# Kernel tuning notes

Hardware: AMD Instinct MI355X
Metric: run time of the kernel (lower is better)

The kernel has to match this reference:

```python
import jax, jax.numpy as jnp
import numpy as np

B, L, K, H = 2, 2048, 48, 128
NUM_IN = 2 * H          # h_E (H) + gathered h_V (H)
SCALE = 30.0            # EncLayer scale
LN_EPS = 1e-5


def _linear_params(key, fan_in, fan_out):
    kw, kb = jax.random.split(key)
    s = 1.0 / np.sqrt(fan_in)
    W = jax.random.uniform(kw, (fan_in, fan_out), minval=-s, maxval=s, dtype=jnp.float32)
    b = jax.random.uniform(kb, (fan_out,), minval=-s, maxval=s, dtype=jnp.float32)
    return W, b


def setup_inputs() -> dict:
    key = jax.random.key(0)
    ks = jax.random.split(key, 12)
    h_V = jax.random.normal(ks[0], (B, L, H), dtype=jnp.float32)
    h_E = jax.random.normal(ks[1], (B, L, K, H), dtype=jnp.float32)
    E_idx = jax.random.randint(ks[2], (B, L, K), 0, L, dtype=jnp.int64)
    mask_V = jnp.ones((B, L), dtype=jnp.float32)
    mask_attend = jnp.ones((B, L, K), dtype=jnp.float32)

    W1, b1 = _linear_params(ks[3], H + NUM_IN, H)
    W2, b2 = _linear_params(ks[4], H, H)
    W3, b3 = _linear_params(ks[5], H, H)
    W11, b11 = _linear_params(ks[6], H + NUM_IN, H)
    W12, b12 = _linear_params(ks[7], H, H)
    W13, b13 = _linear_params(ks[8], H, H)
    Wi, bi = _linear_params(ks[9], H, 4 * H)   # PositionWiseFeedForward W_in
    Wo, bo = _linear_params(ks[10], 4 * H, H)  # W_out

    ln = lambda: (jnp.ones((H,), jnp.float32), jnp.zeros((H,), jnp.float32))
    ln1_s, ln1_b = ln(); ln2_s, ln2_b = ln(); ln3_s, ln3_b = ln()

    return dict(h_V=h_V, h_E=h_E, E_idx=E_idx, mask_V=mask_V, mask_attend=mask_attend,
                W1=W1, b1=b1, W2=W2, b2=b2, W3=W3, b3=b3,
                W11=W11, b11=b11, W12=W12, b12=b12, W13=W13, b13=b13,
                Wi=Wi, bi=bi, Wo=Wo, bo=bo,
                ln1_s=ln1_s, ln1_b=ln1_b, ln2_s=ln2_s, ln2_b=ln2_b,
                ln3_s=ln3_s, ln3_b=ln3_b)


def gather_nodes(nodes, idx):
    # nodes: [B, L, H], idx: [B, L, K] -> [B, L, K, H]
    b, l, h = nodes.shape
    flat = idx.reshape(b, -1)  # [B, L*K]
    g = jnp.take_along_axis(nodes, flat[..., None], axis=1)  # [B, L*K, H]
    return g.reshape(b, idx.shape[1], idx.shape[2], h)


def layer_norm(x, scale, bias):
    mu = jnp.mean(x, axis=-1, keepdims=True)
    var = jnp.mean((x - mu) ** 2, axis=-1, keepdims=True)
    return (x - mu) / jnp.sqrt(var + LN_EPS) * scale + bias


def gelu(x):
    return jax.nn.gelu(x, approximate=False)  # torch nn.GELU default (erf)


def enc_layer_forward(h_V, h_E, E_idx, mask_V, mask_attend, p):
    # --- node update: gather neighbors, concat, MLP, masked sum-reduce ---
    h_EV = jnp.concatenate([h_E, gather_nodes(h_V, E_idx)], axis=-1)        # [B,L,K,2H]
    h_V_exp = jnp.broadcast_to(h_V[:, :, None, :], h_EV.shape[:3] + (h_V.shape[-1],))
    h_EV = jnp.concatenate([h_V_exp, h_EV], axis=-1)                        # [B,L,K,3H]
    m = gelu(h_EV @ p['W1'] + p['b1'])
    m = gelu(m @ p['W2'] + p['b2'])
    m = m @ p['W3'] + p['b3']
    m = mask_attend[..., None] * m
    dh = jnp.sum(m, axis=-2) / SCALE                                        # [B,L,H]
    h_V = layer_norm(h_V + dh, p['ln1_s'], p['ln1_b'])
    # --- position-wise FFN ---
    dh = gelu(h_V @ p['Wi'] + p['bi']) @ p['Wo'] + p['bo']
    h_V = layer_norm(h_V + dh, p['ln2_s'], p['ln2_b'])
    h_V = mask_V[..., None] * h_V
    # --- edge update ---
    h_EV = jnp.concatenate([h_E, gather_nodes(h_V, E_idx)], axis=-1)
    h_V_exp = jnp.broadcast_to(h_V[:, :, None, :], h_EV.shape[:3] + (h_V.shape[-1],))
    h_EV = jnp.concatenate([h_V_exp, h_EV], axis=-1)
    m = gelu(h_EV @ p['W11'] + p['b11'])
    m = gelu(m @ p['W12'] + p['b12'])
    m = m @ p['W13'] + p['b13']
    h_E = layer_norm(h_E + m, p['ln3_s'], p['ln3_b'])
    return h_V, h_E


def reference(h_V, h_E, E_idx, mask_V, mask_attend,
              W1, b1, W2, b2, W3, b3, W11, b11, W12, b12, W13, b13,
              Wi, bi, Wo, bo, ln1_s, ln1_b, ln2_s, ln2_b, ln3_s, ln3_b):
    p = dict(W1=W1, b1=b1, W2=W2, b2=b2, W3=W3, b3=b3,
             W11=W11, b11=b11, W12=W12, b12=b12, W13=W13, b13=b13,
             Wi=Wi, bi=bi, Wo=Wo, bo=bo,
             ln1_s=ln1_s, ln1_b=ln1_b, ln2_s=ln2_s, ln2_b=ln2_b,
             ln3_s=ln3_s, ln3_b=ln3_b)
    return enc_layer_forward(h_V, h_E, E_idx, mask_V, mask_attend, p)
```

## Files before the change

### kernel.cpp

```cpp
#include <hip/hip_runtime.h>
#include <hip/hip_bf16.h>
#include <math.h>

typedef unsigned short u16;
typedef __attribute__((ext_vector_type(8))) short bf16x8;
typedef __attribute__((ext_vector_type(4))) float f32x4;
typedef __attribute__((ext_vector_type(4))) unsigned int uint4v;
typedef __attribute__((ext_vector_type(2))) unsigned int uint2v;
typedef __attribute__((ext_vector_type(4))) unsigned short u16x4;

#define BB 2
#define LL 2048
#define KN 48
#define HH 128
#define NBLK (BB*LL)
#define ST 136

#define WOFF      16
#define OFF_W1MT  (WOFF + 0)
#define OFF_W1ST  (WOFF + 16384)
#define OFF_W1GT  (WOFF + 32768)
#define OFF_W2T   (WOFF + 49152)
#define OFF_W3T   (WOFF + 65536)
#define OFF_W11MT (WOFF + 81920)
#define OFF_W11ST (WOFF + 98304)
#define OFF_W11GT (WOFF + 114688)
#define OFF_W12T  (WOFF + 131072)
#define OFF_W13T  (WOFF + 147456)
#define OFF_WIT   (WOFF + 163840)
#define OFF_WOT   (WOFF + 229376)
#define OFF_HV1   (WOFF + 294912)
#define OFF_Q1    (WOFF + 819200)
#define OFF_Q2    (WOFF + 1343488)
#define OFF_R1    (WOFF + 1867776)
#define OFF_R2    (WOFF + 2916352)
#define PREP_N    294912

__device__ __forceinline__ float b2f(u16 u){
    union { unsigned int i; float f; } v; v.i = ((unsigned int)u) << 16; return v.f;
}
__device__ __forceinline__ u16 f2b(float f){
    unsigned int x = __float_as_uint(f);
    unsigned int r = x + 0x7fffu + ((x >> 16) & 1u);
    return (u16)(r >> 16);
}
__device__ __forceinline__ unsigned int f2b2(float lo, float hi){
    unsigned int r;
    asm("v_cvt_pk_bf16_f32 %0, %1, %2" : "=v"(r) : "v"(lo), "v"(hi));
    return r;
}
__device__ __forceinline__ float gelu_f(float x){
    float ax = fabsf(x) * 0.70710678118654752f;
    float t  = __builtin_amdgcn_rcpf(fmaf(0.3275911f, ax, 1.0f));
    float e  = __builtin_amdgcn_exp2f(ax * ax * -1.4426950408889634f);
    float p  = fmaf(1.061405429f, t, -1.453152027f);
    p = fmaf(p, t, 1.421413741f);
    p = fmaf(p, t, -0.284496736f);
    p = fmaf(p, t, 0.254829592f);
    p = p * t;
    float erfv = fmaf(-p, e, 1.0f);
    float hx = 0.5f * x;
    return fmaf(fabsf(hx), erfv, hx);
}
__device__ __forceinline__ u16 ldb(const void* p, long i, int f32){
    return f32 ? f2b(((const float*)p)[i]) : ((const u16*)p)[i];
}
__device__ __forceinline__ float ldf(const void* p, long i, int f32){
    return f32 ? ((const float*)p)[i] : b2f(((const u16*)p)[i]);
}
__device__ __forceinline__ f32x4 ldf4(const void* p, long i, int f32){
    f32x4 r;
    if (f32){
        r = *(const f32x4*)((const float*)p + i);
    } else {
        u16x4 v = *(const u16x4*)((const u16*)p + i);
        r[0]=b2f(v[0]); r[1]=b2f(v[1]); r[2]=b2f(v[2]); r[3]=b2f(v[3]);
    }
    return r;
}
__device__ __forceinline__ void st4(void* p, long i, f32x4 v, int f32){
    if (f32){
        *(f32x4*)((float*)p + i) = v;
    } else {
        uint2v u; u.x = f2b2(v[0], v[1]); u.y = f2b2(v[2], v[3]);
        *(uint2v*)((u16*)p + i) = u;
    }
}
__device__ __forceinline__ void stage8(u16* dst, const void* src, long off, int f32){
    if (f32){
        const float* s = (const float*)src + off;
        f32x4 a = *(const f32x4*)(s);
        f32x4 b = *(const f32x4*)(s + 4);
        uint4v v;
        v.x = f2b2(a[0], a[1]); v.y = f2b2(a[2], a[3]);
        v.z = f2b2(b[0], b[1]); v.w = f2b2(b[2], b[3]);
        *(uint4v*)dst = v;
    } else {
        *(uint4v*)dst = *(const uint4v*)((const u16*)src + off);
    }
}
__device__ __forceinline__ int ld_idx(const void* p, int i, int i64){
    int v = i64 ? ((const int*)p)[2*i] : ((const int*)p)[i];
    return v & (LL - 1);
}

__global__ void detect_kernel(const void* ln1s, const void* maskV, const void* eidx, int* flags){
    if (threadIdx.x == 0){
        unsigned l0 = ((const unsigned*)ln1s)[0];
        unsigned m0 = ((const unsigned*)maskV)[0];
        int f32 = (l0 == 0x3F800000u || m0 == 0x3F800000u) ? 1 : 0;
        const int* e = (const int*)eidx;
        int orodd = 0, orlow = 0;
        for (int i = 1; i < 64; i += 2) orodd |= e[i];
        for (int i = 0; i < 64; i += 2) orlow |= e[i];
        flags[0] = f32;
        flags[1] = (orodd == 0 && orlow != 0) ? 1 : 0;
    }
}

__global__ void prep_kernel(const void* W1, const void* W2, const void* W3,
                            const void* W11, const void* W12, const void* W13,
                            const void* Wi, const void* Wo, u16* wsbase){
    const int f32 = ((const int*)wsbase)[0];
    int i = blockIdx.x * 256 + threadIdx.x;
    if (i < 16384){ int n = i >> 7, k = i & 127; wsbase[OFF_W1MT + i] = ldb(W1, (128 + k)*128 + n, f32); }
    else if (i < 32768){ int j = i - 16384;  int n = j >> 7, k = j & 127; wsbase[OFF_W1ST  + j] = ldb(W1, k*128 + n, f32); }
    else if (i < 49152){ int j = i - 32768;  int n = j >> 7, k = j & 127; wsbase[OFF_W1GT  + j] = ldb(W1, (256 + k)*128 + n, f32); }
    else if (i < 65536){ int j = i - 49152;  int n = j >> 7, k = j & 127; wsbase[OFF_W2T   + j] = ldb(W2, k*128 + n, f32); }
    else if (i < 81920){ int j = i - 65536;  int n = j >> 7, k = j & 127; wsbase[OFF_W3T   + j] = ldb(W3, k*128 + n, f32); }
    else if (i < 98304){ int j = i - 81920;  int n = j >> 7, k = j & 127; wsbase[OFF_W11MT + j] = ldb(W11, (128 + k)*128 + n, f32); }
    else if (i < 114688){ int j = i - 98304; int n = j >> 7, k = j & 127; wsbase[OFF_W11ST + j] = ldb(W11, k*128 + n, f32); }
    else if (i < 131072){ int j = i - 114688;int n = j >> 7, k = j & 127; wsbase[OFF_W11GT + j] = ldb(W11, (256 + k)*128 + n, f32); }
    else if (i < 147456){ int j = i - 131072;int n = j >> 7, k = j & 127; wsbase[OFF_W12T  + j] = ldb(W12, k*128 + n, f32); }
    else if (i < 163840){ int j = i - 147456;int n = j >> 7, k = j & 127; wsbase[OFF_W13T  + j] = ldb(W13, k*128 + n, f32); }
    else if (i < 229376){ int j = i - 163840; int h = j >> 7, c = j & 127; wsbase[OFF_WIT + j] = ldb(Wi, c*512 + h, f32); }
    else if (i < 294912){ int j = i - 229376; int c = j >> 9, h = j & 511; wsbase[OFF_WOT + j] = ldb(Wo, h*128 + c, f32); }
}

__global__ __launch_bounds__(256) void precomp_kernel(
    const void* __restrict__ src, const void* __restrict__ bias,
    u16* __restrict__ wsbase, long offWs, long offWg, long offQ, long offR)
{
    __shared__ alignas(16) u16 X[16 * ST];
    const int f32 = ((const int*)wsbase)[0];
    const int t = threadIdx.x, lane = t & 63, w = t >> 6;
    const int node0 = blockIdx.x * 16;
    const int r16 = lane & 15, q = lane >> 4, q8 = q * 8;

    {
        int row = t >> 4, ch = t & 15;
        stage8(X + row * ST + ch * 8, src, ((long)(node0 + row)) * HH + ch * 8, f32);
    }
    __syncthreads();

    const u16* bp = X + r16 * ST + q8;
#pragma unroll
    for (int half = 0; half < 2; half++){
        long offW = half ? offWg : offWs;
#pragma unroll
        for (int nt = 0; nt < 2; nt++){
            int wr = w * 32 + nt * 16 + r16;
            const u16* ap = wsbase + offW + (long)wr * 128 + q8;
            f32x4 acc; acc[0]=0.f; acc[1]=0.f; acc[2]=0.f; acc[3]=0.f;
#pragma unroll
            for (int kk = 0; kk < 4; kk++){
                bf16x8 av = *(const bf16x8*)(ap + kk * 32);
                bf16x8 bv = *(const bf16x8*)(bp + kk * 32);
                acc = __builtin_amdgcn_mfma_f32_16x16x32_bf16(av, bv, acc, 0, 0, 0);
            }
            int c0 = w * 32 + nt * 16 + q * 4;
            if (half == 0){
                f32x4 bc = ldf4(bias, c0, f32);
                float* Rf = (float*)(wsbase + offR);
                f32x4 rr; rr[0]=acc[0]+bc[0]; rr[1]=acc[1]+bc[1]; rr[2]=acc[2]+bc[2]; rr[3]=acc[3]+bc[3];
                *(f32x4*)(Rf + (long)(node0 + r16) * HH + c0) = rr;
            } else {
                uint2v u; u.x = f2b2(acc[0], acc[1]); u.y = f2b2(acc[2], acc[3]);
                *(uint2v*)(wsbase + offQ + (long)(node0 + r16) * HH + c0) = u;
            }
        }
    }
}

__device__ __forceinline__ void mfma_WB(const u16* Mls, const bf16x8* W,
                                        f32x4 acc[3], int lane){
    const int r16 = lane & 15;
    const int q8  = (lane >> 4) * 8;
    const u16* bp = Mls + r16 * ST + q8;
#pragma unroll
    for (int kk = 0; kk < 4; kk++){
        bf16x8 b0 = *(const bf16x8*)(bp + kk * 32);
        bf16x8 b1 = *(const bf16x8*)(bp + 16 * ST + kk * 32);
        bf16x8 b2 = *(const bf16x8*)(bp + 32 * ST + kk * 32);
        acc[0] = __builtin_amdgcn_mfma_f32_16x16x32_bf16(W[kk], b0, acc[0], 0, 0, 0);
        acc[1] = __builtin_amdgcn_mfma_f32_16x16x32_bf16(W[kk], b1, acc[1], 0, 0, 0);
        acc[2] = __builtin_amdgcn_mfma_f32_16x16x32_bf16(W[kk], b2, acc[2], 0, 0, 0);
    }
}

__device__ __forceinline__ void zero_acc3(f32x4 acc[3]){
#pragma unroll
    for (int m = 0; m < 3; m++){ acc[m][0]=0.f; acc[m][1]=0.f; acc[m][2]=0.f; acc[m][3]=0.f; }
}

__device__ __forceinline__ void init_accT(f32x4 acc[3], const u16* Qg, int lane, int w){
    const int r16 = lane & 15, q = lane >> 4;
    const int c0 = w * 16 + q * 4;
#pragma unroll
    for (int mt = 0; mt < 3; mt++){
        u16x4 v = *(const u16x4*)(Qg + (mt * 16 + r16) * ST + c0);
        acc[mt][0]=b2f(v[0]); acc[mt][1]=b2f(v[1]); acc[mt][2]=b2f(v[2]); acc[mt][3]=b2f(v[3]);
    }
}

__device__ __forceinline__ void store_T(f32x4 acc[3], u16* M, f32x4 bc4,
                                        int lane, int w, bool dogelu){
    const int r16 = lane & 15, q = lane >> 4;
    const int c0 = w * 16 + q * 4;
#pragma unroll
    for (int mt = 0; mt < 3; mt++){
        float v0 = acc[mt][0] + bc4[0], v1 = acc[mt][1] + bc4[1];
        float v2 = acc[mt][2] + bc4[2], v3 = acc[mt][3] + bc4[3];
        if (dogelu){ v0 = gelu_f(v0); v1 = gelu_f(v1); v2 = gelu_f(v2); v3 = gelu_f(v3); }
        uint2v u; u.x = f2b2(v0, v1); u.y = f2b2(v2, v3);
        *(uint2v*)(M + (mt * 16 + r16) * ST + c0) = u;
    }
}

__global__ __launch_bounds__(512, 6) void node_kernel(
    const void* __restrict__ hV, const void* __restrict__ hE, const void* __restrict__ Eidx,
    const void* __restrict__ maskA,
    const void* __restrict__ b2, const void* __restrict__ b3,
    const void* __restrict__ ln1s, const void* __restrict__ ln1b,
    u16* __restrict__ wsbase)
{
    __shared__ alignas(16) u16 A[KN * ST];
    __shared__ alignas(16) u16 Qg[KN * ST];
    __shared__ alignas(16) u16 M1[KN * ST];
    __shared__ float smask[KN];
    __shared__ alignas(16) float dh[HH];
    __shared__ float hv0f[HH];
    u16* M2 = A;

    const int f32 = ((const int*)wsbase)[0];
    const int i64 = ((const int*)wsbase)[1];
    const u16* ws = wsbase;
    const int t = threadIdx.x, lane = t & 63, w = t >> 6;
    const int bid = blockIdx.x;
    const int b = bid >> 11;
    const int r16 = lane & 15, q = lane >> 4, q8 = q * 8;
    const int wrow = w * 16 + r16;
    const int c0 = w * 16 + q * 4;

    bf16x8 B1[4];
    {
        const u16* bp = ws + OFF_W1MT + (long)wrow * 128 + q8;
#pragma unroll
        for (int k = 0; k < 4; k++) B1[k] = *(const bf16x8*)(bp + k * 32);
    }

    for (int i = t; i < 768; i += 512){
        int row = i >> 4, ch = i & 15;
        stage8(A + row * ST + ch * 8, hE, ((long)bid * KN + row) * HH + ch * 8, f32);
    }
    for (int i = t; i < 768; i += 512){
        int row = i >> 4, ch = i & 15;
        int nb = ld_idx(Eidx, bid * KN + row, i64);
        *(uint4v*)(Qg + row * ST + ch * 8) =
            *(const uint4v*)(ws + OFF_Q1 + ((long)b * LL + nb) * HH + ch * 8);
    }
    if (t < HH) hv0f[t] = ldf(hV, (long)bid * HH + t, f32);
    if (t < KN) smask[t] = ldf(maskA, bid * KN + t, f32);

    bf16x8 B2[4];
    {
        const u16* bp = ws + OFF_W2T + (long)wrow * 128 + q8;
#pragma unroll
        for (int k = 0; k < 4; k++) B2[k] = *(const bf16x8*)(bp + k * 32);
    }
    const f32x4 bc1 = *(const f32x4*)((const float*)(wsbase + OFF_R1) + (long)bid * HH + c0);
    __syncthreads();

    f32x4 acc[3];
    init_accT(acc, Qg, lane, w);
    __builtin_amdgcn_s_setprio(1);
    mfma_WB(A, B1, acc, lane);
    __builtin_amdgcn_s_setprio(0);
    store_T(acc, M1, bc1, lane, w, true);

    bf16x8 B3[4];
    {
        const u16* bp = ws + OFF_W3T + (long)wrow * 128 + q8;
#pragma unroll
        for (int k = 0; k < 4; k++) B3[k] = *(const bf16x8*)(bp + k * 32);
    }
    __syncthreads();

    zero_acc3(acc);
    __builtin_amdgcn_s_setprio(1);
    mfma_WB(M1, B2, acc, lane);
    __builtin_amdgcn_s_setprio(0);
    store_T(acc, M2, ldf4(b2, c0, f32), lane, w, true);
    __syncthreads();

    zero_acc3(acc);
    __builtin_amdgcn_s_setprio(1);
    mfma_WB(M2, B3, acc, lane);
    __builtin_amdgcn_s_setprio(0);

    {
        f32x4 b3v = ldf4(b3, c0, f32);
        f32x4 s; s[0]=0.f; s[1]=0.f; s[2]=0.f; s[3]=0.f;
#pragma unroll
        for (int mt = 0; mt < 3; mt++){
            float mk = smask[mt * 16 + r16];
#pragma unroll
            for (int j = 0; j < 4; j++) s[j] += mk * (acc[mt][j] + b3v[j]);
        }
#pragma unroll
        for (int off = 1; off <= 8; off <<= 1){
#pragma unroll
            for (int j = 0; j < 4; j++) s[j] += __shfl_xor(s[j], off);
        }
        if (r16 == 0) *(f32x4*)&dh[c0] = s;
    }
    __syncthreads();

    if (w == 0){
        float xa = hv0f[lane]      + dh[lane]      * (1.0f / 30.0f);
        float xb = hv0f[64 + lane] + dh[64 + lane] * (1.0f / 30.0f);
        float sum = xa + xb, sq = xa * xa + xb * xb;
#pragma unroll
        for (int off = 1; off < 64; off <<= 1){ sum += __shfl_xor(sum, off); sq += __shfl_xor(sq, off); }
        float mu = sum * (1.0f / 128.0f);
        float var = sq * (1.0f / 128.0f) - mu * mu;
        float rstd = rsqrtf(var + 1e-5f);
        wsbase[OFF_HV1 + (long)bid * HH + lane] =
            f2b((xa - mu) * rstd * ldf(ln1s, lane, f32) + ldf(ln1b, lane, f32));
        wsbase[OFF_HV1 + (long)bid * HH + 64 + lane] =
            f2b((xb - mu) * rstd * ldf(ln1s, 64 + lane, f32) + ldf(ln1b, 64 + lane, f32));
    }
}

__global__ __launch_bounds__(512, 6) void ffn_kernel(
    const void* __restrict__ maskV,
    const void* __restrict__ bi, const void* __restrict__ bo,
    const void* __restrict__ b11,
    const void* __restrict__ ln2s, const void* __restrict__ ln2b,
    u16* __restrict__ wsbase, void* __restrict__ dout)
{
    __shared__ alignas(16) u16 X[16 * 136];
    __shared__ alignas(16) u16 Hid[16 * 520];
    __shared__ alignas(16) float V[16 * 132];

    const int f32 = ((const int*)wsbase)[0];
    const u16* ws = wsbase;
    const u16* hv1 = wsbase + OFF_HV1;
    const int t = threadIdx.x, lane = t & 63, w = t >> 6;
    const int node0 = blockIdx.x * 16;
    const int r16 = lane & 15, q = lane >> 4, q8 = q * 8;
    const int c0 = w * 16 + q * 4;

    if (t < 256){
        int row = t >> 4, ch = t & 15;
        *(uint4v*)(X + row * 136 + ch * 8) =
            *(const uint4v*)(hv1 + (long)(node0 + row) * HH + ch * 8);
    }
    __syncthreads();

    f32x4 acc[4];
#pragma unroll
    for (int nt = 0; nt < 4; nt++){ acc[nt][0]=0.f; acc[nt][1]=0.f; acc[nt][2]=0.f; acc[nt][3]=0.f; }
    {
        const u16* bp = X + r16 * 136 + q8;
#pragma unroll
        for (int kk = 0; kk < 4; kk++){
            bf16x8 bv = *(const bf16x8*)(bp + kk * 32);
#pragma unroll
            for (int nt = 0; nt < 4; nt++){
                const u16* ap = ws + OFF_WIT + (long)(w * 64 + nt * 16 + r16) * 128 + kk * 32 + q8;
                bf16x8 av = *(const bf16x8*)ap;
                acc[nt] = __builtin_amdgcn_mfma_f32_16x16x32_bf16(av, bv, acc[nt], 0, 0, 0);
            }
        }
    }
#pragma unroll
    for (int nt = 0; nt < 4; nt++){
        int hc0 = w * 64 + nt * 16 + q * 4;
        f32x4 bc = ldf4(bi, hc0, f32);
        float g0 = gelu_f(acc[nt][0] + bc[0]), g1 = gelu_f(acc[nt][1] + bc[1]);
        float g2 = gelu_f(acc[nt][2] + bc[2]), g3 = gelu_f(acc[nt][3] + bc[3]);
        uint2v u; u.x = f2b2(g0, g1); u.y = f2b2(g2, g3);
        *(uint2v*)(Hid + r16 * 520 + hc0) = u;
    }
    __syncthreads();

    f32x4 acc2; acc2[0]=0.f; acc2[1]=0.f; acc2[2]=0.f; acc2[3]=0.f;
    {
        const u16* ap = ws + OFF_WOT + (long)(w * 16 + r16) * 512 + q8;
        const u16* bp = Hid + r16 * 520 + q8;
        __builtin_amdgcn_s_setprio(1);
#pragma unroll
        for (int kk = 0; kk < 16; kk++){
            bf16x8 av = *(const bf16x8*)(ap + kk * 32);
            bf16x8 bv = *(const bf16x8*)(bp + kk * 32);
            acc2 = __builtin_amdgcn_mfma_f32_16x16x32_bf16(av, bv, acc2, 0, 0, 0);
        }
        __builtin_amdgcn_s_setprio(0);
    }
    {
        f32x4 bo4 = ldf4(bo, c0, f32);
        u16x4 xr = *(const u16x4*)(X + r16 * 136 + c0);
        f32x4 vv;
        vv[0] = acc2[0] + bo4[0] + b2f(xr[0]);
        vv[1] = acc2[1] + bo4[1] + b2f(xr[1]);
        vv[2] = acc2[2] + bo4[2] + b2f(xr[2]);
        vv[3] = acc2[3] + bo4[3] + b2f(xr[3]);
        *(f32x4*)&V[r16 * 132 + c0] = vv;
    }
    __syncthreads();

    {
        int row = t >> 5, p = t & 31;
        f32x4 v = *(const f32x4*)&V[row * 132 + p * 4];
        float sum = v[0] + v[1] + v[2] + v[3];
        float sq = v[0]*v[0] + v[1]*v[1] + v[2]*v[2] + v[3]*v[3];
#pragma unroll
        for (int off = 1; off < 32; off <<= 1){ sum += __shfl_xor(sum, off); sq += __shfl_xor(sq, off); }
        float mu = sum * (1.0f / 128.0f);
        float var = sq * (1.0f / 128.0f) - mu * mu;
        float rstd = rsqrtf(var + 1e-5f);
        float mv = ldf(maskV, node0 + row, f32);
        f32x4 s4 = ldf4(ln2s, p * 4, f32), bb4 = ldf4(ln2b, p * 4, f32);
        f32x4 y;
#pragma unroll
        for (int j = 0; j < 4; j++) y[j] = ((v[j] - mu) * rstd * s4[j] + bb4[j]) * mv;
        st4(dout, (long)(node0 + row) * HH + p * 4, y, f32);
        uint2v u; u.x = f2b2(y[0], y[1]); u.y = f2b2(y[2], y[3]);
        *(uint2v*)(X + row * 136 + p * 4) = u;
    }
    __syncthreads();

    {
        const u16* bp = X + r16 * 136 + q8;
        f32x4 aR, aQ;
        aR[0]=0.f; aR[1]=0.f; aR[2]=0.f; aR[3]=0.f;
        aQ[0]=0.f; aQ[1]=0.f; aQ[2]=0.f; aQ[3]=0.f;
#pragma unroll
        for (int kk = 0; kk < 4; kk++){
            bf16x8 bv = *(const bf16x8*)(bp + kk * 32);
            bf16x8 avR = *(const bf16x8*)(ws + OFF_W11ST + (long)(w * 16 + r16) * 128 + kk * 32 + q8);
            bf16x8 avQ = *(const bf16x8*)(ws + OFF_W11GT + (long)(w * 16 + r16) * 128 + kk * 32 + q8);
            aR = __builtin_amdgcn_mfma_f32_16x16x32_bf16(avR, bv, aR, 0, 0, 0);
            aQ = __builtin_amdgcn_mfma_f32_16x16x32_bf16(avQ, bv, aQ, 0, 0, 0);
        }
        f32x4 b11v = ldf4(b11, c0, f32);
        float* Rf = (float*)(wsbase + OFF_R2);
        f32x4 rr;
#pragma unroll
        for (int j = 0; j < 4; j++) rr[j] = aR[j] + b11v[j];
        *(f32x4*)(Rf + (long)(node0 + r16) * HH + c0) = rr;
        uint2v u; u.x = f2b2(aQ[0], aQ[1]); u.y = f2b2(aQ[2], aQ[3]);
        *(uint2v*)(wsbase + OFF_Q2 + (long)(node0 + r16) * HH + c0) = u;
    }
}

__global__ __launch_bounds__(512, 6) void edge_kernel(
    const void* __restrict__ hE, const void* __restrict__ Eidx,
    const void* __restrict__ b12, const void* __restrict__ b13,
    const void* __restrict__ ln3s, const void* __restrict__ ln3b,
    u16* __restrict__ wsbase, void* __restrict__ dout)
{
    __shared__ alignas(16) u16 A[KN * ST];
    __shared__ alignas(16) u16 Qg[KN * ST];
    __shared__ alignas(16) u16 M1[KN * ST];
    __shared__ float rowsum[KN];
    __shared__ float rowsq[KN];
    u16* M2 = A;

    const int f32 = ((const int*)wsbase)[0];
    const int i64 = ((const int*)wsbase)[1];
    const u16* ws = wsbase;
    const int t = threadIdx.x, lane = t & 63, w = t >> 6;
    const int bid = blockIdx.x;
    const int b = bid >> 11;
    const int r16 = lane & 15, q = lane >> 4, q8 = q * 8;
    const int wrow = w * 16 + r16;
    const int c0 = w * 16 + q * 4;

    bf16x8 B1[4];
    {
        const u16* bp = ws + OFF_W11MT + (long)wrow * 128 + q8;
#pragma unroll
        for (int k = 0; k < 4; k++) B1[k] = *(const bf16x8*)(bp + k * 32);
    }

    for (int i = t; i < 768; i += 512){
        int row = i >> 4, ch = i & 15;
        stage8(A + row * ST + ch * 8, hE, ((long)bid * KN + row) * HH + ch * 8, f32);
    }
    for (int i = t; i < 768; i += 512){
        int row = i >> 4, ch = i & 15;
        int nb = ld_idx(Eidx, bid * KN + row, i64);
        *(uint4v*)(Qg + row * ST + ch * 8) =
            *(const uint4v*)(ws + OFF_Q2 + ((long)b * LL + nb) * HH + ch * 8);
    }
    if (t < KN){ rowsum[t] = 0.f; rowsq[t] = 0.f; }

    bf16x8 B2[4];
    {
        const u16* bp = ws + OFF_W12T + (long)wrow * 128 + q8;
#pragma unroll
        for (int k = 0; k < 4; k++) B2[k] = *(const bf16x8*)(bp + k * 32);
    }
    const f32x4 bc1 = *(const f32x4*)((const float*)(wsbase + OFF_R2) + (long)bid * HH + c0);
    __syncthreads();

    f32x4 acc[3];
    init_accT(acc, Qg, lane, w);
    __builtin_amdgcn_s_setprio(1);
    mfma_WB(A, B1, acc, lane);
    __builtin_amdgcn_s_setprio(0);
    store_T(acc, M1, bc1, lane, w, true);

    bf16x8 B3[4];
    {
        const u16* bp = ws + OFF_W13T + (long)wrow * 128 + q8;
#pragma unroll
        for (int k = 0; k < 4; k++) B3[k] = *(const bf16x8*)(bp + k * 32);
    }
    __syncthreads();

    zero_acc3(acc);
    __builtin_amdgcn_s_setprio(1);
    mfma_WB(M1, B2, acc, lane);
    __builtin_amdgcn_s_setprio(0);
    store_T(acc, M2, ldf4(b12, c0, f32), lane, w, true);
    __syncthreads();

    zero_acc3(acc);
    __builtin_amdgcn_s_setprio(1);
    mfma_WB(M2, B3, acc, lane);
    __builtin_amdgcn_s_setprio(0);

    f32x4 vals[3];
    {
        f32x4 b13v = ldf4(b13, c0, f32);
#pragma unroll
        for (int mt = 0; mt < 3; mt++){
            int r = mt * 16 + r16;
            f32x4 res = ldf4(hE, ((long)bid * KN + r) * HH + c0, f32);
#pragma unroll
            for (int j = 0; j < 4; j++) vals[mt][j] = acc[mt][j] + b13v[j] + res[j];
        }
    }
    {
        float s[3], ss[3];
#pragma unroll
        for (int mt = 0; mt < 3; mt++){
            s[mt]  = vals[mt][0] + vals[mt][1] + vals[mt][2] + vals[mt][3];
            ss[mt] = vals[mt][0]*vals[mt][0] + vals[mt][1]*vals[mt][1]
                   + vals[mt][2]*vals[mt][2] + vals[mt][3]*vals[mt][3];
            s[mt]  += __shfl_xor(s[mt], 16);  s[mt]  += __shfl_xor(s[mt], 32);
            ss[mt] += __shfl_xor(ss[mt], 16); ss[mt] += __shfl_xor(ss[mt], 32);
        }
        if (lane < 16){
#pragma unroll
            for (int mt = 0; mt < 3; mt++){
                atomicAdd(&rowsum[mt * 16 + lane], s[mt]);
                atomicAdd(&rowsq[mt * 16 + lane], ss[mt]);
            }
        }
    }
    __syncthreads();
    if (t < KN){
        float mu = rowsum[t] * (1.0f / 128.0f);
        float var = rowsq[t] * (1.0f / 128.0f) - mu * mu;
        rowsum[t] = mu;
        rowsq[t] = rsqrtf(var + 1e-5f);
    }
    __syncthreads();

    {
        long ebase = (long)BB * LL * HH;
        f32x4 g4 = ldf4(ln3s, c0, f32), be4 = ldf4(ln3b, c0, f32);
#pragma unroll
        for (int mt = 0; mt < 3; mt++){
            int r = mt * 16 + r16;
            float mu = rowsum[r], rs = rowsq[r];
            f32x4 y;
#pragma unroll
            for (int j = 0; j < 4; j++) y[j] = (vals[mt][j] - mu) * rs * g4[j] + be4[j];
            st4(dout, ebase + ((long)bid * KN + r) * HH + c0, y, f32);
        }
    }
}

extern "C" void kernel_launch(void* const* d_in, const int* in_sizes, int n_in,
                              void* d_out, int out_size, void* d_ws, size_t ws_size,
                              hipStream_t stream) {
    const void* hV    = d_in[0];
    const void* hE    = d_in[1];
    const void* Eidx  = d_in[2];
    const void* maskV = d_in[3];
    const void* maskA = d_in[4];
    const void* W1  = d_in[5];  const void* b1  = d_in[6];
    const void* W2  = d_in[7];  const void* b2  = d_in[8];
    const void* W3  = d_in[9];  const void* b3  = d_in[10];
    const void* W11 = d_in[11]; const void* b11 = d_in[12];
    const void* W12 = d_in[13]; const void* b12 = d_in[14];
    const void* W13 = d_in[15]; const void* b13 = d_in[16];
    const void* Wi  = d_in[17]; const void* bi  = d_in[18];
    const void* Wo  = d_in[19]; const void* bo  = d_in[20];
    const void* ln1s = d_in[21]; const void* ln1b = d_in[22];
    const void* ln2s = d_in[23]; const void* ln2b = d_in[24];
    const void* ln3s = d_in[25]; const void* ln3b = d_in[26];

    u16* ws = (u16*)d_ws;

    detect_kernel<<<1, 64, 0, stream>>>(ln1s, maskV, Eidx, (int*)d_ws);
    prep_kernel<<<(PREP_N + 255) / 256, 256, 0, stream>>>(W1, W2, W3, W11, W12, W13, Wi, Wo, ws);
    precomp_kernel<<<NBLK / 16, 256, 0, stream>>>(hV, b1, ws,
                                                  (long)OFF_W1ST, (long)OFF_W1GT,
                                                  (long)OFF_Q1, (long)OFF_R1);
    node_kernel<<<NBLK, 512, 0, stream>>>(hV, hE, Eidx, maskA,
                                          b2, b3, ln1s, ln1b, ws);
    ffn_kernel<<<NBLK / 16, 512, 0, stream>>>(maskV, bi, bo, b11, ln2s, ln2b, ws, d_out);
    edge_kernel<<<NBLK, 512, 0, stream>>>(hE, Eidx, b12, b13,
                                          ln3s, ln3b, ws, d_out);
}
```

Baseline: 373.1 us.

## Gather neighbor projections directly into accumulators and halve node tiles in small kernels

```diff
diff --git a/kernel.cpp b/kernel.cpp
--- a/kernel.cpp
+++ b/kernel.cpp
@@ -137,19 +137,24 @@
     else if (i < 294912){ int j = i - 229376; int c = j >> 9, h = j & 511; wsbase[OFF_WOT + j] = ldb(Wo, h*128 + c, f32); }
 }
 
-__global__ __launch_bounds__(256) void precomp_kernel(
+__global__ __launch_bounds__(256, 8) void precomp_kernel(
     const void* __restrict__ src, const void* __restrict__ bias,
     u16* __restrict__ wsbase, long offWs, long offWg, long offQ, long offR)
 {
     __shared__ alignas(16) u16 X[16 * ST];
     const int f32 = ((const int*)wsbase)[0];
     const int t = threadIdx.x, lane = t & 63, w = t >> 6;
-    const int node0 = blockIdx.x * 16;
+    const int node0 = blockIdx.x * 8;
     const int r16 = lane & 15, q = lane >> 4, q8 = q * 8;
 
     {
         int row = t >> 4, ch = t & 15;
-        stage8(X + row * ST + ch * 8, src, ((long)(node0 + row)) * HH + ch * 8, f32);
+        if (t < 128){
+            stage8(X + row * ST + ch * 8, src, ((long)(node0 + row)) * HH + ch * 8, f32);
+        } else {
+            uint4v z; z.x=0u; z.y=0u; z.z=0u; z.w=0u;
+            *(uint4v*)(X + row * ST + ch * 8) = z;
+        }
     }
     __syncthreads();
 
@@ -169,14 +174,16 @@
                 acc = __builtin_amdgcn_mfma_f32_16x16x32_bf16(av, bv, acc, 0, 0, 0);
             }
             int c0 = w * 32 + nt * 16 + q * 4;
-            if (half == 0){
-                f32x4 bc = ldf4(bias, c0, f32);
-                float* Rf = (float*)(wsbase + offR);
-                f32x4 rr; rr[0]=acc[0]+bc[0]; rr[1]=acc[1]+bc[1]; rr[2]=acc[2]+bc[2]; rr[3]=acc[3]+bc[3];
-                *(f32x4*)(Rf + (long)(node0 + r16) * HH + c0) = rr;
-            } else {
-                uint2v u; u.x = f2b2(acc[0], acc[1]); u.y = f2b2(acc[2], acc[3]);
-                *(uint2v*)(wsbase + offQ + (long)(node0 + r16) * HH + c0) = u;
+            if (r16 < 8){
+                if (half == 0){
+                    f32x4 bc = ldf4(bias, c0, f32);
+                    float* Rf = (float*)(wsbase + offR);
+                    f32x4 rr; rr[0]=acc[0]+bc[0]; rr[1]=acc[1]+bc[1]; rr[2]=acc[2]+bc[2]; rr[3]=acc[3]+bc[3];
+                    *(f32x4*)(Rf + (long)(node0 + r16) * HH + c0) = rr;
+                } else {
+                    uint2v u; u.x = f2b2(acc[0], acc[1]); u.y = f2b2(acc[2], acc[3]);
+                    *(uint2v*)(wsbase + offQ + (long)(node0 + r16) * HH + c0) = u;
+                }
             }
         }
     }
@@ -203,12 +210,14 @@
     for (int m = 0; m < 3; m++){ acc[m][0]=0.f; acc[m][1]=0.f; acc[m][2]=0.f; acc[m][3]=0.f; }
 }
 
-__device__ __forceinline__ void init_accT(f32x4 acc[3], const u16* Qg, int lane, int w){
+__device__ __forceinline__ void init_accG(f32x4 acc[3], const u16* Qbase, const void* Eidx,
+                                          int bid, int b, int i64, int lane, int w){
     const int r16 = lane & 15, q = lane >> 4;
     const int c0 = w * 16 + q * 4;
 #pragma unroll
     for (int mt = 0; mt < 3; mt++){
-        u16x4 v = *(const u16x4*)(Qg + (mt * 16 + r16) * ST + c0);
+        int nb = ld_idx(Eidx, bid * KN + mt * 16 + r16, i64);
+        u16x4 v = *(const u16x4*)(Qbase + ((long)b * LL + nb) * HH + c0);
         acc[mt][0]=b2f(v[0]); acc[mt][1]=b2f(v[1]); acc[mt][2]=b2f(v[2]); acc[mt][3]=b2f(v[3]);
     }
 }
@@ -235,7 +244,6 @@
     u16* __restrict__ wsbase)
 {
     __shared__ alignas(16) u16 A[KN * ST];
-    __shared__ alignas(16) u16 Qg[KN * ST];
     __shared__ alignas(16) u16 M1[KN * ST];
     __shared__ float smask[KN];
     __shared__ alignas(16) float dh[HH];
@@ -252,6 +260,9 @@
     const int wrow = w * 16 + r16;
     const int c0 = w * 16 + q * 4;
 
+    f32x4 acc[3];
+    init_accG(acc, ws + OFF_Q1, Eidx, bid, b, i64, lane, w);
+
     bf16x8 B1[4];
     {
         const u16* bp = ws + OFF_W1MT + (long)wrow * 128 + q8;
@@ -263,12 +274,6 @@
         int row = i >> 4, ch = i & 15;
         stage8(A + row * ST + ch * 8, hE, ((long)bid * KN + row) * HH + ch * 8, f32);
     }
-    for (int i = t; i < 768; i += 512){
-        int row = i >> 4, ch = i & 15;
-        int nb = ld_idx(Eidx, bid * KN + row, i64);
-        *(uint4v*)(Qg + row * ST + ch * 8) =
-            *(const uint4v*)(ws + OFF_Q1 + ((long)b * LL + nb) * HH + ch * 8);
-    }
     if (t < HH) hv0f[t] = ldf(hV, (long)bid * HH + t, f32);
     if (t < KN) smask[t] = ldf(maskA, bid * KN + t, f32);
 
@@ -281,8 +286,6 @@
     const f32x4 bc1 = *(const f32x4*)((const float*)(wsbase + OFF_R1) + (long)bid * HH + c0);
     __syncthreads();
 
-    f32x4 acc[3];
-    init_accT(acc, Qg, lane, w);
     __builtin_amdgcn_s_setprio(1);
     mfma_WB(A, B1, acc, lane);
     __builtin_amdgcn_s_setprio(0);
@@ -342,7 +345,7 @@
     }
 }
 
-__global__ __launch_bounds__(512, 6) void ffn_kernel(
+__global__ __launch_bounds__(256, 8) void ffn_kernel(
     const void* __restrict__ maskV,
     const void* __restrict__ bi, const void* __restrict__ bo,
     const void* __restrict__ b11,
@@ -357,36 +360,40 @@
     const u16* ws = wsbase;
     const u16* hv1 = wsbase + OFF_HV1;
     const int t = threadIdx.x, lane = t & 63, w = t >> 6;
-    const int node0 = blockIdx.x * 16;
+    const int node0 = blockIdx.x * 8;
     const int r16 = lane & 15, q = lane >> 4, q8 = q * 8;
-    const int c0 = w * 16 + q * 4;
-
-    if (t < 256){
+
+    {
         int row = t >> 4, ch = t & 15;
-        *(uint4v*)(X + row * 136 + ch * 8) =
-            *(const uint4v*)(hv1 + (long)(node0 + row) * HH + ch * 8);
-    }
-    __syncthreads();
-
-    f32x4 acc[4];
-#pragma unroll
-    for (int nt = 0; nt < 4; nt++){ acc[nt][0]=0.f; acc[nt][1]=0.f; acc[nt][2]=0.f; acc[nt][3]=0.f; }
+        if (t < 128){
+            *(uint4v*)(X + row * 136 + ch * 8) =
+                *(const uint4v*)(hv1 + (long)(node0 + row) * HH + ch * 8);
+        } else {
+            uint4v z; z.x=0u; z.y=0u; z.z=0u; z.w=0u;
+            *(uint4v*)(X + row * 136 + ch * 8) = z;
+        }
+    }
+    __syncthreads();
+
+    f32x4 acc[8];
+#pragma unroll
+    for (int nt = 0; nt < 8; nt++){ acc[nt][0]=0.f; acc[nt][1]=0.f; acc[nt][2]=0.f; acc[nt][3]=0.f; }
     {
         const u16* bp = X + r16 * 136 + q8;
 #pragma unroll
         for (int kk = 0; kk < 4; kk++){
             bf16x8 bv = *(const bf16x8*)(bp + kk * 32);
 #pragma unroll
-            for (int nt = 0; nt < 4; nt++){
-                const u16* ap = ws + OFF_WIT + (long)(w * 64 + nt * 16 + r16) * 128 + kk * 32 + q8;
+            for (int nt = 0; nt < 8; nt++){
+                const u16* ap = ws + OFF_WIT + (long)(w * 128 + nt * 16 + r16) * 128 + kk * 32 + q8;
                 bf16x8 av = *(const bf16x8*)ap;
                 acc[nt] = __builtin_amdgcn_mfma_f32_16x16x32_bf16(av, bv, acc[nt], 0, 0, 0);
             }
         }
     }
 #pragma unroll
-    for (int nt = 0; nt < 4; nt++){
-        int hc0 = w * 64 + nt * 16 + q * 4;
+    for (int nt = 0; nt < 8; nt++){
+        int hc0 = w * 128 + nt * 16 + q * 4;
         f32x4 bc = ldf4(bi, hc0, f32);
         float g0 = gelu_f(acc[nt][0] + bc[0]), g1 = gelu_f(acc[nt][1] + bc[1]);
         float g2 = gelu_f(acc[nt][2] + bc[2]), g3 = gelu_f(acc[nt][3] + bc[3]);
@@ -395,28 +402,37 @@
     }
     __syncthreads();
 
-    f32x4 acc2; acc2[0]=0.f; acc2[1]=0.f; acc2[2]=0.f; acc2[3]=0.f;
-    {
-        const u16* ap = ws + OFF_WOT + (long)(w * 16 + r16) * 512 + q8;
-        const u16* bp = Hid + r16 * 520 + q8;
+    f32x4 acc2[2];
+#pragma unroll
+    for (int nt = 0; nt < 2; nt++){ acc2[nt][0]=0.f; acc2[nt][1]=0.f; acc2[nt][2]=0.f; acc2[nt][3]=0.f; }
+    {
+        const u16* bp2 = Hid + r16 * 520 + q8;
         __builtin_amdgcn_s_setprio(1);
 #pragma unroll
         for (int kk = 0; kk < 16; kk++){
-            bf16x8 av = *(const bf16x8*)(ap + kk * 32);
-            bf16x8 bv = *(const bf16x8*)(bp + kk * 32);
-            acc2 = __builtin_amdgcn_mfma_f32_16x16x32_bf16(av, bv, acc2, 0, 0, 0);
+            bf16x8 bv = *(const bf16x8*)(bp2 + kk * 32);
+#pragma unroll
+            for (int nt = 0; nt < 2; nt++){
+                const u16* ap = ws + OFF_WOT + (long)(w * 32 + nt * 16 + r16) * 512 + kk * 32 + q8;
+                bf16x8 av = *(const bf16x8*)ap;
+                acc2[nt] = __builtin_amdgcn_mfma_f32_16x16x32_bf16(av, bv, acc2[nt], 0, 0, 0);
+            }
         }
         __builtin_amdgcn_s_setprio(0);
     }
     {
-        f32x4 bo4 = ldf4(bo, c0, f32);
-        u16x4 xr = *(const u16x4*)(X + r16 * 136 + c0);
-        f32x4 vv;
-        vv[0] = acc2[0] + bo4[0] + b2f(xr[0]);
-        vv[1] = acc2[1] + bo4[1] + b2f(xr[1]);
-        vv[2] = acc2[2] + bo4[2] + b2f(xr[2]);
-        vv[3] = acc2[3] + bo4[3] + b2f(xr[3]);
-        *(f32x4*)&V[r16 * 132 + c0] = vv;
+#pragma unroll
+        for (int nt = 0; nt < 2; nt++){
+            int cc0 = w * 32 + nt * 16 + q * 4;
+            f32x4 bo4 = ldf4(bo, cc0, f32);
+            u16x4 xr = *(const u16x4*)(X + r16 * 136 + cc0);
+            f32x4 vv;
+            vv[0] = acc2[nt][0] + bo4[0] + b2f(xr[0]);
+            vv[1] = acc2[nt][1] + bo4[1] + b2f(xr[1]);
+            vv[2] = acc2[nt][2] + bo4[2] + b2f(xr[2]);
+            vv[3] = acc2[nt][3] + bo4[3] + b2f(xr[3]);
+            *(f32x4*)&V[r16 * 132 + cc0] = vv;
+        }
     }
     __syncthreads();
 
@@ -443,25 +459,32 @@
 
     {
         const u16* bp = X + r16 * 136 + q8;
-        f32x4 aR, aQ;
-        aR[0]=0.f; aR[1]=0.f; aR[2]=0.f; aR[3]=0.f;
-        aQ[0]=0.f; aQ[1]=0.f; aQ[2]=0.f; aQ[3]=0.f;
-#pragma unroll
-        for (int kk = 0; kk < 4; kk++){
-            bf16x8 bv = *(const bf16x8*)(bp + kk * 32);
-            bf16x8 avR = *(const bf16x8*)(ws + OFF_W11ST + (long)(w * 16 + r16) * 128 + kk * 32 + q8);
-            bf16x8 avQ = *(const bf16x8*)(ws + OFF_W11GT + (long)(w * 16 + r16) * 128 + kk * 32 + q8);
-            aR = __builtin_amdgcn_mfma_f32_16x16x32_bf16(avR, bv, aR, 0, 0, 0);
-            aQ = __builtin_amdgcn_mfma_f32_16x16x32_bf16(avQ, bv, aQ, 0, 0, 0);
-        }
-        f32x4 b11v = ldf4(b11, c0, f32);
-        float* Rf = (float*)(wsbase + OFF_R2);
-        f32x4 rr;
-#pragma unroll
-        for (int j = 0; j < 4; j++) rr[j] = aR[j] + b11v[j];
-        *(f32x4*)(Rf + (long)(node0 + r16) * HH + c0) = rr;
-        uint2v u; u.x = f2b2(aQ[0], aQ[1]); u.y = f2b2(aQ[2], aQ[3]);
-        *(uint2v*)(wsbase + OFF_Q2 + (long)(node0 + r16) * HH + c0) = u;
+#pragma unroll
+        for (int nt = 0; nt < 2; nt++){
+            int wr = w * 32 + nt * 16 + r16;
+            f32x4 aR, aQ;
+            aR[0]=0.f; aR[1]=0.f; aR[2]=0.f; aR[3]=0.f;
+            aQ[0]=0.f; aQ[1]=0.f; aQ[2]=0.f; aQ[3]=0.f;
+#pragma unroll
+            for (int kk = 0; kk < 4; kk++){
+                bf16x8 bv = *(const bf16x8*)(bp + kk * 32);
+                bf16x8 avR = *(const bf16x8*)(ws + OFF_W11ST + (long)wr * 128 + kk * 32 + q8);
+                bf16x8 avQ = *(const bf16x8*)(ws + OFF_W11GT + (long)wr * 128 + kk * 32 + q8);
+                aR = __builtin_amdgcn_mfma_f32_16x16x32_bf16(avR, bv, aR, 0, 0, 0);
+                aQ = __builtin_amdgcn_mfma_f32_16x16x32_bf16(avQ, bv, aQ, 0, 0, 0);
+            }
+            if (r16 < 8){
+                int cc0 = w * 32 + nt * 16 + q * 4;
+                f32x4 b11v = ldf4(b11, cc0, f32);
+                float* Rf = (float*)(wsbase + OFF_R2);
+                f32x4 rr;
+#pragma unroll
+                for (int j = 0; j < 4; j++) rr[j] = aR[j] + b11v[j];
+                *(f32x4*)(Rf + (long)(node0 + r16) * HH + cc0) = rr;
+                uint2v u; u.x = f2b2(aQ[0], aQ[1]); u.y = f2b2(aQ[2], aQ[3]);
+                *(uint2v*)(wsbase + OFF_Q2 + (long)(node0 + r16) * HH + cc0) = u;
+            }
+        }
     }
 }
 
@@ -472,7 +495,6 @@
     u16* __restrict__ wsbase, void* __restrict__ dout)
 {
     __shared__ alignas(16) u16 A[KN * ST];
-    __shared__ alignas(16) u16 Qg[KN * ST];
     __shared__ alignas(16) u16 M1[KN * ST];
     __shared__ float rowsum[KN];
     __shared__ float rowsq[KN];
@@ -488,6 +510,9 @@
     const int wrow = w * 16 + r16;
     const int c0 = w * 16 + q * 4;
 
+    f32x4 acc[3];
+    init_accG(acc, ws + OFF_Q2, Eidx, bid, b, i64, lane, w);
+
     bf16x8 B1[4];
     {
         const u16* bp = ws + OFF_W11MT + (long)wrow * 128 + q8;
@@ -499,12 +524,6 @@
         int row = i >> 4, ch = i & 15;
         stage8(A + row * ST + ch * 8, hE, ((long)bid * KN + row) * HH + ch * 8, f32);
     }
-    for (int i = t; i < 768; i += 512){
-        int row = i >> 4, ch = i & 15;
-        int nb = ld_idx(Eidx, bid * KN + row, i64);
-        *(uint4v*)(Qg + row * ST + ch * 8) =
-            *(const uint4v*)(ws + OFF_Q2 + ((long)b * LL + nb) * HH + ch * 8);
-    }
     if (t < KN){ rowsum[t] = 0.f; rowsq[t] = 0.f; }
 
     bf16x8 B2[4];
@@ -516,8 +535,6 @@
     const f32x4 bc1 = *(const f32x4*)((const float*)(wsbase + OFF_R2) + (long)bid * HH + c0);
     __syncthreads();
 
-    f32x4 acc[3];
-    init_accT(acc, Qg, lane, w);
     __builtin_amdgcn_s_setprio(1);
     mfma_WB(A, B1, acc, lane);
     __builtin_amdgcn_s_setprio(0);
@@ -620,12 +637,12 @@
 
     detect_kernel<<<1, 64, 0, stream>>>(ln1s, maskV, Eidx, (int*)d_ws);
     prep_kernel<<<(PREP_N + 255) / 256, 256, 0, stream>>>(W1, W2, W3, W11, W12, W13, Wi, Wo, ws);
-    precomp_kernel<<<NBLK / 16, 256, 0, stream>>>(hV, b1, ws,
-                                                  (long)OFF_W1ST, (long)OFF_W1GT,
-                                                  (long)OFF_Q1, (long)OFF_R1);
+    precomp_kernel<<<NBLK / 8, 256, 0, stream>>>(hV, b1, ws,
+                                                 (long)OFF_W1ST, (long)OFF_W1GT,
+                                                 (long)OFF_Q1, (long)OFF_R1);
     node_kernel<<<NBLK, 512, 0, stream>>>(hV, hE, Eidx, maskA,
                                           b2, b3, ln1s, ln1b, ws);
-    ffn_kernel<<<NBLK / 16, 512, 0, stream>>>(maskV, bi, bo, b11, ln2s, ln2b, ws, d_out);
+    ffn_kernel<<<NBLK / 8, 256, 0, stream>>>(maskV, bi, bo, b11, ln2s, ln2b, ws, d_out);
     edge_kernel<<<NBLK, 512, 0, stream>>>(hE, Eidx, b12, b13,
                                           ln3s, ln3b, ws, d_out);
 }
```

After: 389.5 us. 4.4% more time.

## Hoist W3 past masked neighbor sum and alias shared buffers

Applied to the files above, without the earlier changes.

```diff
diff --git a/kernel.cpp b/kernel.cpp
--- a/kernel.cpp
+++ b/kernel.cpp
@@ -104,24 +104,22 @@
     return v & (LL - 1);
 }
 
-__global__ void detect_kernel(const void* ln1s, const void* maskV, const void* eidx, int* flags){
-    if (threadIdx.x == 0){
-        unsigned l0 = ((const unsigned*)ln1s)[0];
-        unsigned m0 = ((const unsigned*)maskV)[0];
-        int f32 = (l0 == 0x3F800000u || m0 == 0x3F800000u) ? 1 : 0;
+__global__ void prep_kernel(const void* W1, const void* W2, const void* W3,
+                            const void* W11, const void* W12, const void* W13,
+                            const void* Wi, const void* Wo,
+                            const void* ln1s, const void* maskV, const void* eidx,
+                            u16* wsbase){
+    unsigned l0 = ((const unsigned*)ln1s)[0];
+    unsigned m0 = ((const unsigned*)maskV)[0];
+    const int f32 = (l0 == 0x3F800000u || m0 == 0x3F800000u) ? 1 : 0;
+    if (blockIdx.x == 0 && threadIdx.x == 0){
         const int* e = (const int*)eidx;
         int orodd = 0, orlow = 0;
         for (int i = 1; i < 64; i += 2) orodd |= e[i];
         for (int i = 0; i < 64; i += 2) orlow |= e[i];
-        flags[0] = f32;
-        flags[1] = (orodd == 0 && orlow != 0) ? 1 : 0;
-    }
-}
-
-__global__ void prep_kernel(const void* W1, const void* W2, const void* W3,
-                            const void* W11, const void* W12, const void* W13,
-                            const void* Wi, const void* Wo, u16* wsbase){
-    const int f32 = ((const int*)wsbase)[0];
+        ((int*)wsbase)[0] = f32;
+        ((int*)wsbase)[1] = (orodd == 0 && orlow != 0) ? 1 : 0;
+    }
     int i = blockIdx.x * 256 + threadIdx.x;
     if (i < 16384){ int n = i >> 7, k = i & 127; wsbase[OFF_W1MT + i] = ldb(W1, (128 + k)*128 + n, f32); }
     else if (i < 32768){ int j = i - 16384;  int n = j >> 7, k = j & 127; wsbase[OFF_W1ST  + j] = ldb(W1, k*128 + n, f32); }
@@ -236,11 +234,11 @@
 {
     __shared__ alignas(16) u16 A[KN * ST];
     __shared__ alignas(16) u16 Qg[KN * ST];
-    __shared__ alignas(16) u16 M1[KN * ST];
     __shared__ float smask[KN];
+    __shared__ alignas(16) float sL[HH];
     __shared__ alignas(16) float dh[HH];
     __shared__ float hv0f[HH];
-    u16* M2 = A;
+    u16* M1 = Qg;
 
     const int f32 = ((const int*)wsbase)[0];
     const int i64 = ((const int*)wsbase)[1];
@@ -287,42 +285,52 @@
     mfma_WB(A, B1, acc, lane);
     __builtin_amdgcn_s_setprio(0);
     store_T(acc, M1, bc1, lane, w, true);
-
-    bf16x8 B3[4];
-    {
-        const u16* bp = ws + OFF_W3T + (long)wrow * 128 + q8;
-#pragma unroll
-        for (int k = 0; k < 4; k++) B3[k] = *(const bf16x8*)(bp + k * 32);
-    }
     __syncthreads();
 
     zero_acc3(acc);
     __builtin_amdgcn_s_setprio(1);
     mfma_WB(M1, B2, acc, lane);
     __builtin_amdgcn_s_setprio(0);
-    store_T(acc, M2, ldf4(b2, c0, f32), lane, w, true);
-    __syncthreads();
-
-    zero_acc3(acc);
-    __builtin_amdgcn_s_setprio(1);
-    mfma_WB(M2, B3, acc, lane);
-    __builtin_amdgcn_s_setprio(0);
-
-    {
-        f32x4 b3v = ldf4(b3, c0, f32);
+
+    float cnt;
+    {
+        f32x4 b2v = ldf4(b2, c0, f32);
         f32x4 s; s[0]=0.f; s[1]=0.f; s[2]=0.f; s[3]=0.f;
+        float cm = smask[r16] + smask[16 + r16] + smask[32 + r16];
 #pragma unroll
         for (int mt = 0; mt < 3; mt++){
             float mk = smask[mt * 16 + r16];
 #pragma unroll
-            for (int j = 0; j < 4; j++) s[j] += mk * (acc[mt][j] + b3v[j]);
+            for (int j = 0; j < 4; j++)
+                s[j] += mk * gelu_f(acc[mt][j] + b2v[j]);
         }
 #pragma unroll
         for (int off = 1; off <= 8; off <<= 1){
 #pragma unroll
             for (int j = 0; j < 4; j++) s[j] += __shfl_xor(s[j], off);
-        }
-        if (r16 == 0) *(f32x4*)&dh[c0] = s;
+            cm += __shfl_xor(cm, off);
+        }
+        cnt = cm;
+        if (r16 == 0) *(f32x4*)&sL[c0] = s;
+    }
+    __syncthreads();
+
+    {
+        int n = t >> 2, p = t & 3;
+        const u16* wr = ws + OFF_W3T + (long)n * 128 + p * 32;
+        float a = 0.f;
+#pragma unroll
+        for (int cc = 0; cc < 8; cc++){
+            u16x4 wv = *(const u16x4*)(wr + cc * 4);
+            f32x4 sv = *(const f32x4*)&sL[p * 32 + cc * 4];
+            a = fmaf(b2f(wv[0]), sv[0], a);
+            a = fmaf(b2f(wv[1]), sv[1], a);
+            a = fmaf(b2f(wv[2]), sv[2], a);
+            a = fmaf(b2f(wv[3]), sv[3], a);
+        }
+        a += __shfl_xor(a, 1);
+        a += __shfl_xor(a, 2);
+        if (p == 0) dh[n] = a + cnt * ldf(b3, n, f32);
     }
     __syncthreads();
 
@@ -473,9 +481,9 @@
 {
     __shared__ alignas(16) u16 A[KN * ST];
     __shared__ alignas(16) u16 Qg[KN * ST];
-    __shared__ alignas(16) u16 M1[KN * ST];
     __shared__ float rowsum[KN];
     __shared__ float rowsq[KN];
+    u16* M1 = Qg;
     u16* M2 = A;
 
     const int f32 = ((const int*)wsbase)[0];
@@ -618,8 +626,8 @@
 
     u16* ws = (u16*)d_ws;
 
-    detect_kernel<<<1, 64, 0, stream>>>(ln1s, maskV, Eidx, (int*)d_ws);
-    prep_kernel<<<(PREP_N + 255) / 256, 256, 0, stream>>>(W1, W2, W3, W11, W12, W13, Wi, Wo, ws);
+    prep_kernel<<<(PREP_N + 255) / 256, 256, 0, stream>>>(W1, W2, W3, W11, W12, W13, Wi, Wo,
+                                                          ln1s, maskV, Eidx, ws);
     precomp_kernel<<<NBLK / 16, 256, 0, stream>>>(hV, b1, ws,
                                                   (long)OFF_W1ST, (long)OFF_W1GT,
                                                   (long)OFF_Q1, (long)OFF_R1);
```

Measured after the change: 370.3 us. Within noise of the previous version (-0.8%).
